# Performance work log

Measured on AMD Instinct MI355X. Metric: run time of the kernel, lower is better.

The kernel has to match this reference:

```python
import jax, jax.numpy as jnp
import numpy as np
import math

COV_WEIGHT = 1.0
BANDWIDTH_FACTOR = 1.06
SQRT_2PI = math.sqrt(2.0 * math.pi)
EPS_LOG = 1e-8
H_MIN = 1e-4


def setup_inputs() -> dict:
    key = jax.random.key(0)
    activity = jax.random.normal(key, (2048, 64), dtype=jnp.float32)
    return {"activity": activity}


def reference(activity):
    B, R = activity.shape
    # Silverman bandwidth per receptor (torch .std uses ddof=1)
    std = jnp.std(activity, axis=0, ddof=1)                     # (R,)
    h = jnp.maximum(BANDWIDTH_FACTOR * std * (B ** (-0.2)), H_MIN)  # (R,)

    # Pairwise Gaussian KDE: query == samples == activity
    u = (activity[:, None, :] - activity[None, :, :]) / h       # (B_q, B_s, R)
    kernel_values = jnp.exp(-0.5 * u * u) / SQRT_2PI             # (B_q, B_s, R)
    density = kernel_values.sum(axis=1) / (B * h)                # (B_q, R)

    entropies = -jnp.mean(jnp.log(density + EPS_LOG), axis=0)    # (R,)
    loss_entropy = -entropies.mean()

    # Covariance penalty: sum of squared off-diagonals
    centered = activity - activity.mean(axis=0, keepdims=True)
    cov = (centered.T @ centered) / (B - 1)                      # (R, R)
    off = cov - jnp.diag(jnp.diag(cov))
    loss_cov = jnp.sum(off * off)

    total_loss = loss_entropy + COV_WEIGHT * loss_cov
    return total_loss
```

## Files before the change

kernel.cpp:

```cpp
#include <hip/hip_runtime.h>
#include <math.h>

#define B_SZ 2048
#define R_SZ 64
#define QT 8
#define KDE_BLOCKS (B_SZ / QT)

#define B_POW_NEG02 0.217637640824031f
#define SQRT_2PI 2.5066282746310002f
#define LOG2E 1.44269504088896340736f

extern "C" __device__ float __ocml_native_exp2_f32(float);

typedef __attribute__((ext_vector_type(2))) float f32x2;


__global__ __launch_bounds__(1024) void cov_stats_kernel(const float* __restrict__ A,
                                                         float* __restrict__ U,
                                                         float* __restrict__ lscale,
                                                         float* __restrict__ cov_partial,
                                                         float* __restrict__ ent_acc,
                                                         int* __restrict__ done_cnt) {
    int i = blockIdx.x;
    int tid = threadIdx.x;
    int j = tid & 63, bg = tid >> 6;

    float g = 0.f, sj = 0.f, s2j = 0.f;
#pragma unroll 4
    for (int b = bg; b < B_SZ; b += 16) {
        float ai = A[b * R_SZ + i];
        float aj = A[b * R_SZ + j];
        g = fmaf(ai, aj, g);
        sj += aj;
        s2j = fmaf(aj, aj, s2j);
    }

    __shared__ float gred[16][64], sred[16][64], s2red[16][64];
    __shared__ float gfin[64], sfin[64], hs[64];
    gred[bg][j] = g; sred[bg][j] = sj; s2red[bg][j] = s2j;
    __syncthreads();
    if (tid < 64) {
        float G = 0.f, S = 0.f, S2 = 0.f;
#pragma unroll
        for (int t = 0; t < 16; ++t) { G += gred[t][j]; S += sred[t][j]; S2 += s2red[t][j]; }
        gfin[j] = G;
        sfin[j] = S;
        float m = S * (1.f / (float)B_SZ);
        float var = (S2 - S * m) * (1.f / (float)(B_SZ - 1));
        var = fmaxf(var, 0.f);
        float h = fmaxf(1.06f * sqrtf(var) * B_POW_NEG02, 1e-4f);
        hs[j] = sqrtf(0.5f * LOG2E) / h;
        if (i == 0) lscale[j] = 1.0f / ((float)B_SZ * h * SQRT_2PI);
    }
    __syncthreads();
    if (tid < 64) {
        float m_j = sfin[j] * (1.f / (float)B_SZ);
        float m_i = sfin[i] * (1.f / (float)B_SZ);
        float cov = (gfin[j] - (float)B_SZ * m_i * m_j) * (1.f / (float)(B_SZ - 1));
        float v = (j == i) ? 0.f : cov * cov;
        for (int off = 32; off > 0; off >>= 1) v += __shfl_down(v, off, 64);
        if (j == 0) cov_partial[i] = v;
    }
    if (i == 0 && tid == 64) { *ent_acc = 0.f; *done_cnt = 0; }

    int base = i * (32 * R_SZ);
    float k0 = hs[tid & 63];
    U[base + tid]        = A[base + tid]        * k0;
    U[base + 1024 + tid] = A[base + 1024 + tid] * k0;
}

__global__ __launch_bounds__(1024) void kde_kernel(const float* __restrict__ U,
                                                   const float* __restrict__ lscale,
                                                   const float* __restrict__ cov_partial,
                                                   float* __restrict__ ent_acc,
                                                   int* __restrict__ done_cnt,
                                                   float* __restrict__ out) {
    int tid = threadIdx.x;
    int r = tid & 63, sg = tid >> 6;
    int q0 = blockIdx.x * QT;

    f32x2 uq01 = { U[(q0 + 0) * R_SZ + r], U[(q0 + 1) * R_SZ + r] };
    f32x2 uq23 = { U[(q0 + 2) * R_SZ + r], U[(q0 + 3) * R_SZ + r] };
    f32x2 uq45 = { U[(q0 + 4) * R_SZ + r], U[(q0 + 5) * R_SZ + r] };
    f32x2 uq67 = { U[(q0 + 6) * R_SZ + r], U[(q0 + 7) * R_SZ + r] };
    f32x2 c01 = { 0.f, 0.f }, c23 = { 0.f, 0.f };
    f32x2 c45 = { 0.f, 0.f }, c67 = { 0.f, 0.f };

#pragma unroll 4
    for (int s = sg; s < B_SZ; s += 16) {
        float us = U[s * R_SZ + r];
        f32x2 uss = { us, us };
        f32x2 d01 = uq01 - uss, d23 = uq23 - uss;
        f32x2 d45 = uq45 - uss, d67 = uq67 - uss;
        f32x2 n01 = -d01 * d01, n23 = -d23 * d23;
        f32x2 n45 = -d45 * d45, n67 = -d67 * d67;
        f32x2 e01 = { __ocml_native_exp2_f32(n01.x), __ocml_native_exp2_f32(n01.y) };
        f32x2 e23 = { __ocml_native_exp2_f32(n23.x), __ocml_native_exp2_f32(n23.y) };
        f32x2 e45 = { __ocml_native_exp2_f32(n45.x), __ocml_native_exp2_f32(n45.y) };
        f32x2 e67 = { __ocml_native_exp2_f32(n67.x), __ocml_native_exp2_f32(n67.y) };
        c01 += e01; c23 += e23; c45 += e45; c67 += e67;
    }

    __shared__ float red[16][QT][64];
    red[sg][0][r] = c01.x; red[sg][1][r] = c01.y;
    red[sg][2][r] = c23.x; red[sg][3][r] = c23.y;
    red[sg][4][r] = c45.x; red[sg][5][r] = c45.y;
    red[sg][6][r] = c67.x; red[sg][7][r] = c67.y;
    __syncthreads();
    __shared__ float wred[QT];
    if (sg < QT) {
        float S = 0.f;
#pragma unroll
        for (int t = 0; t < 16; ++t) S += red[t][sg][r];
        float v = __logf(fmaf(S, lscale[r], 1e-8f));
        for (int off = 32; off > 0; off >>= 1) v += __shfl_down(v, off, 64);
        if (r == 0) wred[sg] = v;
    }
    __syncthreads();
    __shared__ int lastflag;
    if (tid == 0) {
        float p = 0.f;
#pragma unroll
        for (int t = 0; t < QT; ++t) p += wred[t];
        p *= (1.0f / ((float)B_SZ * (float)R_SZ));
        atomicAdd(ent_acc, p);
        __threadfence();
        int prev = atomicAdd(done_cnt, 1);
        lastflag = (prev == KDE_BLOCKS - 1);
    }
    __syncthreads();
    if (lastflag && tid < 64) {
        __threadfence();
        float v = cov_partial[tid];
        for (int off = 32; off > 0; off >>= 1) v += __shfl_down(v, off, 64);
        if (tid == 0) {
            float ent = __hip_atomic_load(ent_acc, __ATOMIC_ACQUIRE,
                                          __HIP_MEMORY_SCOPE_AGENT);
            out[0] = ent + v;
        }
    }
}

extern "C" void kernel_launch(void* const* d_in, const int* in_sizes, int n_in,
                              void* d_out, int out_size, void* d_ws, size_t ws_size,
                              hipStream_t stream) {
    const float* A = (const float*)d_in[0];
    float* out = (float*)d_out;

    float* wsf = (float*)d_ws;
    float* lscale      = wsf;
    float* cov_partial = wsf + 64;
    float* ent_acc     = wsf + 160;
    int*   done_cnt    = (int*)(wsf + 192);
    float* U           = wsf + 256;

    cov_stats_kernel<<<R_SZ, 1024, 0, stream>>>(A, U, lscale, cov_partial,
                                                ent_acc, done_cnt);
    kde_kernel<<<KDE_BLOCKS, 1024, 0, stream>>>(U, lscale, cov_partial,
                                                ent_acc, done_cnt, out);
}
```

Before: 103.3 us.

## Exploit kernel symmetry to halve pairwise KDE exp evaluations

The pairwise Gaussian kernel is symmetric, so each query block now evaluates only about half the sample rows, using a circular window of the next 1024 rows. Each exp value is credited both to the query's row sum and, through an atomic add, to the sample row's density buffer. A third kernel then takes the logs and does the final reduction. This roughly halves the exp and arithmetic work, at the cost of many global float atomics, an extra launch, and a density buffer that must be zeroed.

```diff
diff --git a/kernel.cpp b/kernel.cpp
--- a/kernel.cpp
+++ b/kernel.cpp
@@ -3,8 +3,9 @@
 
 #define B_SZ 2048
 #define R_SZ 64
-#define QT 8
-#define KDE_BLOCKS (B_SZ / QT)
+#define QB 8
+#define NB (B_SZ / QB)
+#define IDX_MASK (B_SZ * R_SZ - 1)
 
 #define B_POW_NEG02 0.217637640824031f
 #define SQRT_2PI 2.5066282746310002f
@@ -17,10 +18,11 @@
 
 __global__ __launch_bounds__(1024) void cov_stats_kernel(const float* __restrict__ A,
                                                          float* __restrict__ U,
+                                                         float* __restrict__ density,
                                                          float* __restrict__ lscale,
                                                          float* __restrict__ cov_partial,
                                                          float* __restrict__ ent_acc,
-                                                         int* __restrict__ done_cnt) {
+                                                         int* __restrict__ done2) {
     int i = blockIdx.x;
     int tid = threadIdx.x;
     int j = tid & 63, bg = tid >> 6;
@@ -61,82 +63,120 @@
         for (int off = 32; off > 0; off >>= 1) v += __shfl_down(v, off, 64);
         if (j == 0) cov_partial[i] = v;
     }
-    if (i == 0 && tid == 64) { *ent_acc = 0.f; *done_cnt = 0; }
+    if (i == 0 && tid == 64) { *ent_acc = 0.f; *done2 = 0; }
 
     int base = i * (32 * R_SZ);
     float k0 = hs[tid & 63];
     U[base + tid]        = A[base + tid]        * k0;
     U[base + 1024 + tid] = A[base + 1024 + tid] * k0;
-}
-
-__global__ __launch_bounds__(1024) void kde_kernel(const float* __restrict__ U,
-                                                   const float* __restrict__ lscale,
-                                                   const float* __restrict__ cov_partial,
-                                                   float* __restrict__ ent_acc,
-                                                   int* __restrict__ done_cnt,
-                                                   float* __restrict__ out) {
+    density[base + tid] = 0.f;
+    density[base + 1024 + tid] = 0.f;
+}
+
+__global__ __launch_bounds__(1024) void kde_sym_kernel(const float* __restrict__ U,
+                                                       float* __restrict__ density) {
     int tid = threadIdx.x;
     int r = tid & 63, sg = tid >> 6;
-    int q0 = blockIdx.x * QT;
+    int t = blockIdx.x;
+    int q0 = t * QB;
 
     f32x2 uq01 = { U[(q0 + 0) * R_SZ + r], U[(q0 + 1) * R_SZ + r] };
     f32x2 uq23 = { U[(q0 + 2) * R_SZ + r], U[(q0 + 3) * R_SZ + r] };
     f32x2 uq45 = { U[(q0 + 4) * R_SZ + r], U[(q0 + 5) * R_SZ + r] };
     f32x2 uq67 = { U[(q0 + 6) * R_SZ + r], U[(q0 + 7) * R_SZ + r] };
-    f32x2 c01 = { 0.f, 0.f }, c23 = { 0.f, 0.f };
-    f32x2 c45 = { 0.f, 0.f }, c67 = { 0.f, 0.f };
-
-#pragma unroll 4
-    for (int s = sg; s < B_SZ; s += 16) {
-        float us = U[s * R_SZ + r];
+    f32x2 r01 = {0.f,0.f}, r23 = {0.f,0.f}, r45 = {0.f,0.f}, r67 = {0.f,0.f};
+
+    if (sg == 0) {
+#pragma unroll
+        for (int i = 0; i < QB; ++i) {
+            float us = U[(q0 + i) * R_SZ + r];
+            f32x2 uss = { us, us };
+            f32x2 d01 = uq01 - uss, d23 = uq23 - uss;
+            f32x2 d45 = uq45 - uss, d67 = uq67 - uss;
+            f32x2 n01 = -d01*d01, n23 = -d23*d23, n45 = -d45*d45, n67 = -d67*d67;
+            f32x2 e01 = { __ocml_native_exp2_f32(n01.x), __ocml_native_exp2_f32(n01.y) };
+            f32x2 e23 = { __ocml_native_exp2_f32(n23.x), __ocml_native_exp2_f32(n23.y) };
+            f32x2 e45 = { __ocml_native_exp2_f32(n45.x), __ocml_native_exp2_f32(n45.y) };
+            f32x2 e67 = { __ocml_native_exp2_f32(n67.x), __ocml_native_exp2_f32(n67.y) };
+            r01 += e01; r23 += e23; r45 += e45; r67 += e67;
+        }
+    }
+
+    int niter = (sg == 15 && t >= NB / 2) ? 56 : 64;
+    int row0 = (q0 + 8 + 64 * sg) & (B_SZ - 1);
+    int idx0 = row0 * R_SZ + r;
+    int li = idx0;
+    float p0 = U[li]; li = (li + R_SZ) & IDX_MASK;
+    float p1 = U[li]; li = (li + R_SZ) & IDX_MASK;
+    int ui = idx0;
+    for (int i = 0; i < niter; ++i) {
+        float us = p0; p0 = p1;
+        p1 = U[li];
+        li = (li + R_SZ) & IDX_MASK;
         f32x2 uss = { us, us };
         f32x2 d01 = uq01 - uss, d23 = uq23 - uss;
         f32x2 d45 = uq45 - uss, d67 = uq67 - uss;
-        f32x2 n01 = -d01 * d01, n23 = -d23 * d23;
-        f32x2 n45 = -d45 * d45, n67 = -d67 * d67;
+        f32x2 n01 = -d01*d01, n23 = -d23*d23, n45 = -d45*d45, n67 = -d67*d67;
         f32x2 e01 = { __ocml_native_exp2_f32(n01.x), __ocml_native_exp2_f32(n01.y) };
         f32x2 e23 = { __ocml_native_exp2_f32(n23.x), __ocml_native_exp2_f32(n23.y) };
         f32x2 e45 = { __ocml_native_exp2_f32(n45.x), __ocml_native_exp2_f32(n45.y) };
         f32x2 e67 = { __ocml_native_exp2_f32(n67.x), __ocml_native_exp2_f32(n67.y) };
-        c01 += e01; c23 += e23; c45 += e45; c67 += e67;
-    }
-
-    __shared__ float red[16][QT][64];
-    red[sg][0][r] = c01.x; red[sg][1][r] = c01.y;
-    red[sg][2][r] = c23.x; red[sg][3][r] = c23.y;
-    red[sg][4][r] = c45.x; red[sg][5][r] = c45.y;
-    red[sg][6][r] = c67.x; red[sg][7][r] = c67.y;
-    __syncthreads();
-    __shared__ float wred[QT];
-    if (sg < QT) {
+        r01 += e01; r23 += e23; r45 += e45; r67 += e67;
+        f32x2 t0 = e01 + e23, t1 = e45 + e67;
+        f32x2 t2 = t0 + t1;
+        unsafeAtomicAdd(&density[ui], t2.x + t2.y);
+        ui = (ui + R_SZ) & IDX_MASK;
+    }
+
+    __shared__ float red[16][QB][64];
+    red[sg][0][r] = r01.x; red[sg][1][r] = r01.y;
+    red[sg][2][r] = r23.x; red[sg][3][r] = r23.y;
+    red[sg][4][r] = r45.x; red[sg][5][r] = r45.y;
+    red[sg][6][r] = r67.x; red[sg][7][r] = r67.y;
+    __syncthreads();
+    if (sg < QB) {
         float S = 0.f;
 #pragma unroll
-        for (int t = 0; t < 16; ++t) S += red[t][sg][r];
-        float v = __logf(fmaf(S, lscale[r], 1e-8f));
-        for (int off = 32; off > 0; off >>= 1) v += __shfl_down(v, off, 64);
-        if (r == 0) wred[sg] = v;
-    }
+        for (int w = 0; w < 16; ++w) S += red[w][sg][r];
+        unsafeAtomicAdd(&density[(q0 + sg) * R_SZ + r], S);
+    }
+}
+
+__global__ __launch_bounds__(1024) void entropy_kernel(const float* __restrict__ density,
+                                                       const float* __restrict__ lscale,
+                                                       const float* __restrict__ cov_partial,
+                                                       float* __restrict__ ent_acc,
+                                                       int* __restrict__ done2,
+                                                       float* __restrict__ out) {
+    int tid = threadIdx.x;
+    int r = tid & 63, sg = tid >> 6;
+    float ls = lscale[r];
+    int f = blockIdx.x * 2048 + tid;
+    float v = __logf(fmaf(density[f], ls, 1e-8f))
+            + __logf(fmaf(density[f + 1024], ls, 1e-8f));
+    for (int off = 32; off > 0; off >>= 1) v += __shfl_down(v, off, 64);
+    __shared__ float wr[16];
+    if (r == 0) wr[sg] = v;
     __syncthreads();
     __shared__ int lastflag;
     if (tid == 0) {
-        float p = 0.f;
-#pragma unroll
-        for (int t = 0; t < QT; ++t) p += wred[t];
-        p *= (1.0f / ((float)B_SZ * (float)R_SZ));
-        atomicAdd(ent_acc, p);
+        float s = 0.f;
+#pragma unroll
+        for (int w = 0; w < 16; ++w) s += wr[w];
+        atomicAdd(ent_acc, s);
         __threadfence();
-        int prev = atomicAdd(done_cnt, 1);
-        lastflag = (prev == KDE_BLOCKS - 1);
+        int prev = atomicAdd(done2, 1);
+        lastflag = (prev == 63);
     }
     __syncthreads();
     if (lastflag && tid < 64) {
         __threadfence();
-        float v = cov_partial[tid];
-        for (int off = 32; off > 0; off >>= 1) v += __shfl_down(v, off, 64);
+        float v2 = cov_partial[tid];
+        for (int off = 32; off > 0; off >>= 1) v2 += __shfl_down(v2, off, 64);
         if (tid == 0) {
             float ent = __hip_atomic_load(ent_acc, __ATOMIC_ACQUIRE,
                                           __HIP_MEMORY_SCOPE_AGENT);
-            out[0] = ent + v;
+            out[0] = ent * (1.0f / ((float)B_SZ * (float)R_SZ)) + v2;
         }
     }
 }
@@ -151,11 +191,13 @@
     float* lscale      = wsf;
     float* cov_partial = wsf + 64;
     float* ent_acc     = wsf + 160;
-    int*   done_cnt    = (int*)(wsf + 192);
+    int*   done2       = (int*)(wsf + 192);
     float* U           = wsf + 256;
-
-    cov_stats_kernel<<<R_SZ, 1024, 0, stream>>>(A, U, lscale, cov_partial,
-                                                ent_acc, done_cnt);
-    kde_kernel<<<KDE_BLOCKS, 1024, 0, stream>>>(U, lscale, cov_partial,
-                                                ent_acc, done_cnt, out);
-}
+    float* density     = wsf + 256 + B_SZ * R_SZ;
+
+    cov_stats_kernel<<<R_SZ, 1024, 0, stream>>>(A, U, density, lscale, cov_partial,
+                                                ent_acc, done2);
+    kde_sym_kernel<<<NB, 1024, 0, stream>>>(U, density);
+    entropy_kernel<<<64, 1024, 0, stream>>>(density, lscale, cov_partial,
+                                            ent_acc, done2, out);
+}
```

Result: slower. 128.0 us (+23.9%).
